# Performance work log

Hardware: AMD Instinct MI355X
Metric: run time of the kernel (lower is better)

## Reference

```python
import jax, jax.numpy as jnp
import numpy as np
import math

B, T, H, W, D = 64, 512, 128, 128, 32


def _lin(k, out, inn):
    k1, k2 = jax.random.split(k)
    lim = 1.0 / np.sqrt(inn)
    return (jax.random.uniform(k1, (out, inn), jnp.float32, -lim, lim),
            jax.random.uniform(k2, (out,), jnp.float32, -lim, lim))


def setup_inputs() -> dict:
    key = jax.random.key(0)
    ks = jax.random.split(key, 12)
    ts = jnp.broadcast_to(jnp.linspace(0.0, 4.0 * math.pi, T, dtype=jnp.float32), (B, T))
    coef = lambda k: jax.random.normal(k, (B, T - 1, D), jnp.float32) * 0.1
    i_W0, i_b0 = _lin(ks[4], W, D)
    i_W1, i_b1 = _lin(ks[5], W, W)
    i_W2, i_b2 = _lin(ks[6], H, W)
    f_W0, f_b0 = _lin(ks[7], W, H)
    f_W1, f_b1 = _lin(ks[8], W, W)
    f_W2, f_b2 = _lin(ks[9], H * D, W)
    l_W, l_b = _lin(ks[10], 1, H)
    return dict(ts=ts,
                coeff_d=coef(ks[0]), coeff_c=coef(ks[1]), coeff_b=coef(ks[2]), coeff_a=coef(ks[3]),
                i_W0=i_W0, i_b0=i_b0, i_W1=i_W1, i_b1=i_b1, i_W2=i_W2, i_b2=i_b2,
                f_W0=f_W0, f_b0=f_b0, f_W1=f_W1, f_b1=f_b1, f_W2=f_W2, f_b2=f_b2,
                l_W=l_W, l_b=l_b)


def reference(ts, coeff_d, coeff_c, coeff_b, coeff_a,
              i_W0, i_b0, i_W1, i_b1, i_W2, i_b2,
              f_W0, f_b0, f_W1, f_b1, f_W2, f_b2,
              l_W, l_b):
    def initial_mlp(x):  # eqx.nn.MLP default: relu hidden, identity final
        x = jax.nn.relu(i_W0 @ x + i_b0)
        x = jax.nn.relu(i_W1 @ x + i_b1)
        return i_W2 @ x + i_b2

    def func_mlp(y):  # softplus hidden, tanh final, reshape (H, D)
        h = jax.nn.softplus(f_W0 @ y + f_b0)
        h = jax.nn.softplus(f_W1 @ h + f_b1)
        return jnp.tanh(f_W2 @ h + f_b2).reshape(H, D)

    def single(ts_i, d, c, b, a):
        dt = ts_i[1] - ts_i[0]
        y0 = initial_mlp(a[0])  # control.evaluate(ts[0]) = a[0] (frac=0 in first interval)

        def deriv(t):  # diffrax CubicInterpolation.derivative
            idx = jnp.clip(jnp.searchsorted(ts_i, t, side='right') - 1, 0, ts_i.shape[0] - 2)
            frac = t - ts_i[idx]
            return b[idx] + frac * (2.0 * c[idx] + frac * 3.0 * d[idx])

        def f(t, y):  # ControlTerm.to_ode() vf_prod with control=dt
            return (func_mlp(y) @ deriv(t)) * dt

        def step(carry, _):  # ralston_step_fn
            t0, y = carry
            k1 = f(t0, y)
            k2 = f(t0 + 0.5 * dt, y + 0.5 * k1)
            k3 = f(t0 + 0.75 * dt, y + 0.75 * k2)
            y1 = (2.0 / 9.0 * k1 + 1.0 / 3.0 * k2 + 4.0 / 9.0 * k3) * dt + y
            return (t0 + dt, y1), y1

        _, ys = jax.lax.scan(step, (ts_i[0], y0), None, length=ts_i.shape[0])
        return jax.nn.sigmoid(ys @ l_W[0] + l_b[0])  # (T,), evolving_out=True

    return jax.vmap(single)(ts, coeff_d, coeff_c, coeff_b, coeff_a)
```

## Files before the change

kernel.cpp:

```cpp
#include <hip/hip_runtime.h>
#include <hip/hip_bf16.h>

#define TT 512
#define BB 64
#define HH 128
#define WW 128
#define DD 32
#define NTHR 512
#define CSTRIDE 16352

#define SMEM_BYTES 86016

typedef __attribute__((ext_vector_type(8))) short short8;
typedef __attribute__((ext_vector_type(4))) float f32x4;

__device__ __forceinline__ float softplus_f(float x) {
    return fmaxf(x, 0.f) + __logf(1.f + __expf(-fabsf(x)));
}
__device__ __forceinline__ float fast_tanh(float x) {
    float ax = fabsf(x);
    float e  = __expf(-2.f * ax);
    float r  = (1.f - e) * __builtin_amdgcn_rcpf(1.f + e);
    return copysignf(r, x);
}
__device__ __forceinline__ short bf16rne(float x) {
    unsigned u = __float_as_uint(x);
    u += 0x7fffu + ((u >> 16) & 1u);
    return (short)(u >> 16);
}
__device__ __forceinline__ void store_l2(unsigned long long* p, unsigned long long v) {
    asm volatile("global_store_dwordx2 %0, %1, off sc0"
                 :: "v"(p), "v"(v) : "memory");
}
__device__ __forceinline__ unsigned long long load_l2_atomic(unsigned long long* p) {
    unsigned long long v;
    asm volatile("global_atomic_add_x2 %0, %1, %2, off sc0\n\t"
                 "s_waitcnt vmcnt(0)"
                 : "=v"(v) : "v"(p), "v"(0ULL) : "memory");
    return v;
}

__global__ __launch_bounds__(NTHR, 2)
void cde_kernel(const float* __restrict__ ts,
                const float* __restrict__ cd, const float* __restrict__ cc,
                const float* __restrict__ cb, const float* __restrict__ ca,
                const float* __restrict__ iW0, const float* __restrict__ ib0,
                const float* __restrict__ iW1, const float* __restrict__ ib1,
                const float* __restrict__ iW2, const float* __restrict__ ib2,
                const float* __restrict__ fW0, const float* __restrict__ fb0,
                const float* __restrict__ fW1, const float* __restrict__ fb1,
                const float* __restrict__ fW2, const float* __restrict__ fb2,
                const float* __restrict__ lW, const float* __restrict__ lb,
                unsigned* __restrict__ xcdctr,
                float* camb,
                unsigned long long* kslow,
                float* __restrict__ out)
{
    extern __shared__ float sm[];
    float* tss    = sm;
    float* ybuf   = tss + TT;
    float* dvec   = ybuf + 128;
    float* scr    = dvec + 96;
    short* ybf    = (short*)(scr + 256);
    short* h1bf   = ybf + 128;
    short* h2bf   = h1bf + 128;
    int*   clm    = (int*)(h2bf + 128);

    const int tid  = threadIdx.x;
    const int lane = tid & 63;
    const int wv   = tid >> 6;
    const int quad = lane >> 4;
    const int qr   = lane & 15;

    if (tid == 0) {
        unsigned xcc;
        asm volatile("s_getreg_b32 %0, hwreg(HW_REG_XCC_ID)" : "=s"(xcc));
        xcc &= 7u;
        unsigned slot = atomicAdd(&xcdctr[xcc], 1u);
        clm[0] = (int)(xcc * 8u + (slot >> 2));
        clm[1] = (int)(slot & 3u);
    }
    __syncthreads();
    const int b = clm[0];
    const int m = clm[1];

    unsigned long long* kfast =
        (unsigned long long*)(camb + (size_t)b * CSTRIDE + 2048);

    const int cg = qr & 3;
    const int ct = (qr >> 2) & 1;
    const int rh = qr >> 3;
    const int dbase = ct * 16 + quad * 4 + rh * 2;

    for (int i = tid; i < TT; i += NTHR) tss[i] = ts[(size_t)b * TT + i];

    short8 afr[4][8];
    #pragma unroll
    for (int gi = 0; gi < 4; ++gi) {
        int g = m * 32 + wv * 4 + gi;
        #pragma unroll
        for (int t = 0; t < 2; ++t)
        #pragma unroll
        for (int K = 0; K < 4; ++K) {
            int row = g * 32 + t * 16 + qr;
            int col = K * 32 + quad * 8;
            const float* src = fW2 + (size_t)row * WW + col;
            short8 v;
            #pragma unroll
            for (int j = 0; j < 8; ++j) v[j] = bf16rne(src[j]);
            afr[gi][t * 4 + K] = v;
        }
    }
    short8 w0f[4], w1f[4];
    #pragma unroll
    for (int K = 0; K < 4; ++K) {
        int row = wv * 16 + qr;
        int col = K * 32 + quad * 8;
        const float* s0 = fW0 + (size_t)row * HH + col;
        const float* s1 = fW1 + (size_t)row * WW + col;
        short8 v0, v1;
        #pragma unroll
        for (int j = 0; j < 8; ++j) { v0[j] = bf16rne(s0[j]); v1[j] = bf16rne(s1[j]); }
        w0f[K] = v0; w1f[K] = v1;
    }
    const float fb0r = fb0[wv * 16 + quad * 4 + cg];
    const float fb1r = fb1[wv * 16 + quad * 4 + cg];
    const int   hrow = m * 32 + wv * 4 + cg;
    const float fb2a = fb2[hrow * 32 + dbase];
    const float fb2b = fb2[hrow * 32 + dbase + 1];

    __syncthreads();

    const float dt = tss[1] - tss[0];
    float t00 = tss[0];
    const size_t cstride = (size_t)CSTRIDE;
    const float* cdb = cd + (size_t)b * cstride;
    const float* ccb = cc + (size_t)b * cstride;
    const float* cbb = cb + (size_t)b * cstride;

    if (tid < HH) {
        const float* a0 = ca + (size_t)b * cstride;
        float acc = ib0[tid];
        #pragma unroll
        for (int k = 0; k < DD; ++k) acc += iW0[tid * DD + k] * a0[k];
        scr[tid] = fmaxf(acc, 0.f);
    }
    __syncthreads();
    if (tid < HH) {
        float acc = ib1[tid];
        for (int k = 0; k < WW; ++k) acc += iW1[tid * WW + k] * scr[k];
        scr[128 + tid] = fmaxf(acc, 0.f);
    }
    __syncthreads();
    float yreg = 0.f, k1r = 0.f, k2r = 0.f;
    if (tid < HH) {
        float acc = ib2[tid];
        for (int k = 0; k < WW; ++k) acc += iW2[tid * WW + k] * scr[128 + k];
        yreg = acc;
        ybuf[tid] = acc;
        ybf[tid]  = bf16rne(acc);
    }
    __syncthreads();

    float lwa = 0.f, lwb = 0.f, lbv = 0.f;
    if (wv == 0) { lwa = lW[lane]; lwb = lW[64 + lane]; lbv = lb[0]; }

    for (int s = 0; s < TT; ++s) {
        if (wv < 3) {
            float tv = t00 + ((wv == 0) ? 0.f : (wv == 1) ? 0.5f : 0.75f) * dt;
            int cnt = 0;
            #pragma unroll
            for (int ch = 0; ch < 8; ++ch)
                cnt += __popcll(__ballot(tss[ch * 64 + lane] <= tv));
            int idx = min(max(cnt - 1, 0), TT - 2);
            if (lane < DD) {
                float frac = tv - tss[idx];
                size_t o = (size_t)idx * DD + lane;
                dvec[wv * 32 + lane] =
                    cbb[o] + frac * (2.f * ccb[o] + frac * 3.f * cdb[o]);
            }
        }

        #pragma unroll 1
        for (int q = 0; q < 3; ++q) {
            const int gen = s * 3 + q + 1;
            const int buf = gen & 1;

            {
                f32x4 aA = {0.f, 0.f, 0.f, 0.f}, aB = {0.f, 0.f, 0.f, 0.f};
                short8 b0 = *(const short8*)(ybf + 0 * 32 + quad * 8);
                short8 b1 = *(const short8*)(ybf + 1 * 32 + quad * 8);
                short8 b2 = *(const short8*)(ybf + 2 * 32 + quad * 8);
                short8 b3 = *(const short8*)(ybf + 3 * 32 + quad * 8);
                aA = __builtin_amdgcn_mfma_f32_16x16x32_bf16(w0f[0], b0, aA, 0, 0, 0);
                aB = __builtin_amdgcn_mfma_f32_16x16x32_bf16(w0f[1], b1, aB, 0, 0, 0);
                aA = __builtin_amdgcn_mfma_f32_16x16x32_bf16(w0f[2], b2, aA, 0, 0, 0);
                aB = __builtin_amdgcn_mfma_f32_16x16x32_bf16(w0f[3], b3, aB, 0, 0, 0);
                f32x4 h = aA + aB;
                if (qr < 4) {
                    float v = (qr & 1) ? ((qr & 2) ? h[3] : h[1])
                                       : ((qr & 2) ? h[2] : h[0]);
                    h1bf[wv * 16 + quad * 4 + qr] = bf16rne(softplus_f(v + fb0r));
                }
            }
            __syncthreads();
            {
                f32x4 aA = {0.f, 0.f, 0.f, 0.f}, aB = {0.f, 0.f, 0.f, 0.f};
                short8 b0 = *(const short8*)(h1bf + 0 * 32 + quad * 8);
                short8 b1 = *(const short8*)(h1bf + 1 * 32 + quad * 8);
                short8 b2 = *(const short8*)(h1bf + 2 * 32 + quad * 8);
                short8 b3 = *(const short8*)(h1bf + 3 * 32 + quad * 8);
                aA = __builtin_amdgcn_mfma_f32_16x16x32_bf16(w1f[0], b0, aA, 0, 0, 0);
                aB = __builtin_amdgcn_mfma_f32_16x16x32_bf16(w1f[1], b1, aB, 0, 0, 0);
                aA = __builtin_amdgcn_mfma_f32_16x16x32_bf16(w1f[2], b2, aA, 0, 0, 0);
                aB = __builtin_amdgcn_mfma_f32_16x16x32_bf16(w1f[3], b3, aB, 0, 0, 0);
                f32x4 h = aA + aB;
                if (qr < 4) {
                    float v = (qr & 1) ? ((qr & 2) ? h[3] : h[1])
                                       : ((qr & 2) ? h[2] : h[0]);
                    h2bf[wv * 16 + quad * 4 + qr] = bf16rne(softplus_f(v + fb1r));
                }
            }
            __syncthreads();
            {
                short8 bfr[4];
                #pragma unroll
                for (int K = 0; K < 4; ++K)
                    bfr[K] = *(const short8*)(h2bf + K * 32 + quad * 8);
                f32x4 A0[4], A1[4];
                #pragma unroll
                for (int gi = 0; gi < 4; ++gi) {
                    f32x4 a0 = {0.f, 0.f, 0.f, 0.f};
                    f32x4 a1 = {0.f, 0.f, 0.f, 0.f};
                    a0 = __builtin_amdgcn_mfma_f32_16x16x32_bf16(afr[gi][0], bfr[0], a0, 0, 0, 0);
                    a0 = __builtin_amdgcn_mfma_f32_16x16x32_bf16(afr[gi][1], bfr[1], a0, 0, 0, 0);
                    a0 = __builtin_amdgcn_mfma_f32_16x16x32_bf16(afr[gi][2], bfr[2], a0, 0, 0, 0);
                    a0 = __builtin_amdgcn_mfma_f32_16x16x32_bf16(afr[gi][3], bfr[3], a0, 0, 0, 0);
                    a1 = __builtin_amdgcn_mfma_f32_16x16x32_bf16(afr[gi][4], bfr[0], a1, 0, 0, 0);
                    a1 = __builtin_amdgcn_mfma_f32_16x16x32_bf16(afr[gi][5], bfr[1], a1, 0, 0, 0);
                    a1 = __builtin_amdgcn_mfma_f32_16x16x32_bf16(afr[gi][6], bfr[2], a1, 0, 0, 0);
                    a1 = __builtin_amdgcn_mfma_f32_16x16x32_bf16(afr[gi][7], bfr[3], a1, 0, 0, 0);
                    A0[gi] = a0; A1[gi] = a1;
                }
                f32x4 s0a = (cg & 1) ? A0[1] : A0[0];
                f32x4 s0b = (cg & 1) ? A0[3] : A0[2];
                f32x4 s0  = (cg & 2) ? s0b : s0a;
                f32x4 s1a = (cg & 1) ? A1[1] : A1[0];
                f32x4 s1b = (cg & 1) ? A1[3] : A1[2];
                f32x4 s1  = (cg & 2) ? s1b : s1a;
                f32x4 st  = ct ? s1 : s0;
                float va = rh ? st[2] : st[0];
                float vb = rh ? st[3] : st[1];
                float2 dv = *(const float2*)(dvec + q * 32 + dbase);
                float p = fast_tanh(va + fb2a) * dv.x + fast_tanh(vb + fb2b) * dv.y;
                p += __shfl_xor(p, 8);
                p += __shfl_xor(p, 4);
                p += __shfl_xor(p, 16);
                p += __shfl_xor(p, 32);
                if (lane < 4) {
                    const float kval = p * dt;
                    const size_t off = (size_t)buf * HH + m * 32 + wv * 4 + lane;
                    unsigned long long pk =
                        ((unsigned long long)__float_as_uint(kval) << 32) | (unsigned)gen;
                    store_l2(kfast + off, pk);
                    __hip_atomic_store(&kslow[(size_t)(buf * BB + b) * HH + m * 32 + wv * 4 + lane],
                                       pk, __ATOMIC_RELAXED, __HIP_MEMORY_SCOPE_AGENT);
                }
            }

            if (tid < HH) {
                unsigned long long* fp = kfast + (size_t)buf * HH + tid;
                unsigned long long v;
                int it = 0;
                for (;;) {
                    if (it < 8 || (it & 1) == 0) {
                        v = load_l2_atomic(fp);
                    } else {
                        v = __hip_atomic_load(&kslow[(size_t)(buf * BB + b) * HH + tid],
                                              __ATOMIC_RELAXED, __HIP_MEMORY_SCOPE_AGENT);
                    }
                    if ((unsigned)v == (unsigned)gen) break;
                    if (++it > 64) __builtin_amdgcn_s_sleep(1);
                }
                float kv = __uint_as_float((unsigned)(v >> 32));
                float nxt;
                if (q == 0)      { k1r = kv; nxt = yreg + 0.5f  * kv; }
                else if (q == 1) { k2r = kv; nxt = yreg + 0.75f * kv; }
                else {
                    nxt = yreg + dt * ((2.f/9.f) * k1r + (1.f/3.f) * k2r + (4.f/9.f) * kv);
                    yreg = nxt;
                    ybuf[tid] = nxt;
                }
                ybf[tid] = bf16rne(nxt);
            }
            __syncthreads();
        }

        if (m == 0 && wv == 0) {
            float p = ybuf[lane] * lwa + ybuf[64 + lane] * lwb;
            p += __shfl_xor(p, 1);  p += __shfl_xor(p, 2);  p += __shfl_xor(p, 4);
            p += __shfl_xor(p, 8);  p += __shfl_xor(p, 16); p += __shfl_xor(p, 32);
            if (lane == 0) out[(size_t)b * TT + s] = 1.f / (1.f + __expf(-(p + lbv)));
        }
        t00 += dt;
    }
}

extern "C" void kernel_launch(void* const* d_in, const int* in_sizes, int n_in,
                              void* d_out, int out_size, void* d_ws, size_t ws_size,
                              hipStream_t stream) {
    const float* ts  = (const float*)d_in[0];
    const float* cdp = (const float*)d_in[1];
    const float* ccp = (const float*)d_in[2];
    const float* cbp = (const float*)d_in[3];
    const float* cap = (const float*)d_in[4];
    const float* iW0 = (const float*)d_in[5];
    const float* ib0 = (const float*)d_in[6];
    const float* iW1 = (const float*)d_in[7];
    const float* ib1 = (const float*)d_in[8];
    const float* iW2 = (const float*)d_in[9];
    const float* ib2 = (const float*)d_in[10];
    const float* fW0 = (const float*)d_in[11];
    const float* fb0 = (const float*)d_in[12];
    const float* fW1 = (const float*)d_in[13];
    const float* fb1 = (const float*)d_in[14];
    const float* fW2 = (const float*)d_in[15];
    const float* fb2 = (const float*)d_in[16];
    const float* lW  = (const float*)d_in[17];
    const float* lb  = (const float*)d_in[18];
    float* out = (float*)d_out;

    unsigned* xcdctr = (unsigned*)d_ws;
    unsigned long long* kslow = (unsigned long long*)((char*)d_ws + 256);
    hipMemsetAsync(d_ws, 0, 256 + (size_t)2 * BB * HH * sizeof(unsigned long long), stream);

    hipFuncSetAttribute((const void*)cde_kernel,
                        hipFuncAttributeMaxDynamicSharedMemorySize, SMEM_BYTES);
    hipLaunchKernelGGL(cde_kernel, dim3(256), dim3(NTHR), SMEM_BYTES, stream,
                       ts, cdp, ccp, cbp, cap, iW0, ib0, iW1, ib1, iW2, ib2,
                       fW0, fb0, fW1, fb1, fW2, fb2, lW, lb, xcdctr,
                       (float*)cap, kslow, out);
}
```

Baseline: 3.606 ms.

## Carry first-layer pre-activation state instead of y and exchange partial projections

The solver state becomes z = W0·y + b0 instead of y. Because z is linear in y, each Ralston stage updates z with W0·k, computed as per-block partial sums over each block's 32-row slice of k. The blocks exchange these partials all-to-all through L2 and poll the three peer slots at once. This removes the first-layer MFMA and its barrier from every stage, and the logistic readout is built the same way by accumulating lW·k partials. In exchange each stage adds a 32-wide fp32 dot, three-way polling with more memory traffic, a new barrier for the local k buffer, and a larger workspace.

```diff
diff --git a/kernel.cpp b/kernel.cpp
--- a/kernel.cpp
+++ b/kernel.cpp
@@ -38,6 +38,13 @@
                  "s_waitcnt vmcnt(0)"
                  : "=v"(v) : "v"(p), "v"(0ULL) : "memory");
     return v;
+}
+__device__ __forceinline__ void probe_issue(unsigned long long* p, unsigned long long& v) {
+    asm volatile("global_atomic_add_x2 %0, %1, %2, off sc0"
+                 : "=v"(v) : "v"(p), "v"(0ULL) : "memory");
+}
+__device__ __forceinline__ void probe_collect(unsigned long long& v) {
+    asm volatile("s_waitcnt vmcnt(0)" : "+v"(v) :: "memory");
 }
 
 __global__ __launch_bounds__(NTHR, 2)
@@ -61,8 +68,8 @@
     float* ybuf   = tss + TT;
     float* dvec   = ybuf + 128;
     float* scr    = dvec + 96;
-    short* ybf    = (short*)(scr + 256);
-    short* h1bf   = ybf + 128;
+    float* klocal = scr + 256;
+    short* h1bf   = (short*)(klocal + 32);
     short* h2bf   = h1bf + 128;
     int*   clm    = (int*)(h2bf + 128);
 
@@ -84,8 +91,10 @@
     const int b = clm[0];
     const int m = clm[1];
 
-    unsigned long long* kfast =
-        (unsigned long long*)(camb + (size_t)b * CSTRIDE + 2048);
+    unsigned long long* ufast = (unsigned long long*)(camb + (size_t)b * CSTRIDE + 2048);
+    unsigned long long* sfast = ufast + (size_t)2 * HH * 4;
+    unsigned long long* umirror = kslow;
+    unsigned long long* smirror = kslow + (size_t)2 * BB * HH * 4;
 
     const int cg = qr & 3;
     const int ct = (qr >> 2) & 1;
@@ -111,23 +120,32 @@
             afr[gi][t * 4 + K] = v;
         }
     }
-    short8 w0f[4], w1f[4];
+    short8 w1f[4];
     #pragma unroll
     for (int K = 0; K < 4; ++K) {
         int row = wv * 16 + qr;
         int col = K * 32 + quad * 8;
-        const float* s0 = fW0 + (size_t)row * HH + col;
         const float* s1 = fW1 + (size_t)row * WW + col;
-        short8 v0, v1;
-        #pragma unroll
-        for (int j = 0; j < 8; ++j) { v0[j] = bf16rne(s0[j]); v1[j] = bf16rne(s1[j]); }
-        w0f[K] = v0; w1f[K] = v1;
-    }
-    const float fb0r = fb0[wv * 16 + quad * 4 + cg];
+        short8 v1;
+        #pragma unroll
+        for (int j = 0; j < 8; ++j) v1[j] = bf16rne(s1[j]);
+        w1f[K] = v1;
+    }
+    float W0s[32];
+    if (tid < HH) {
+        #pragma unroll
+        for (int j = 0; j < 32; ++j) W0s[j] = fW0[(size_t)tid * HH + m * 32 + j];
+    } else {
+        #pragma unroll
+        for (int j = 0; j < 32; ++j) W0s[j] = 0.f;
+    }
     const float fb1r = fb1[wv * 16 + quad * 4 + cg];
     const int   hrow = m * 32 + wv * 4 + cg;
     const float fb2a = fb2[hrow * 32 + dbase];
     const float fb2b = fb2[hrow * 32 + dbase + 1];
+    float lwa = 0.f, lwb = 0.f, lbv = 0.f, lWs = 0.f;
+    if (wv == 3) { lwa = lW[lane]; lwb = lW[64 + lane]; lbv = lb[0]; }
+    if (wv == 7 && lane < 32) lWs = lW[m * 32 + lane];
 
     __syncthreads();
 
@@ -152,18 +170,30 @@
         scr[128 + tid] = fmaxf(acc, 0.f);
     }
     __syncthreads();
-    float yreg = 0.f, k1r = 0.f, k2r = 0.f;
     if (tid < HH) {
         float acc = ib2[tid];
         for (int k = 0; k < WW; ++k) acc += iW2[tid * WW + k] * scr[128 + k];
-        yreg = acc;
         ybuf[tid] = acc;
-        ybf[tid]  = bf16rne(acc);
-    }
-    __syncthreads();
-
-    float lwa = 0.f, lwb = 0.f, lbv = 0.f;
-    if (wv == 0) { lwa = lW[lane]; lwb = lW[64 + lane]; lbv = lb[0]; }
+    }
+    __syncthreads();
+
+    float zb = 0.f, U1r = 0.f, U2r = 0.f;
+    if (tid < HH) {
+        float acc = fb0[tid];
+        for (int k = 0; k < WW; ++k) acc += fW0[(size_t)tid * HH + k] * ybuf[k];
+        zb = acc;
+        h1bf[tid] = bf16rne(softplus_f(acc));
+    }
+    float rreg = 0.f;
+    if (wv == 3) {
+        float p = ybuf[lane] * lwa + ybuf[64 + lane] * lwb;
+        p += __shfl_xor(p, 1);  p += __shfl_xor(p, 2);  p += __shfl_xor(p, 4);
+        p += __shfl_xor(p, 8);  p += __shfl_xor(p, 16); p += __shfl_xor(p, 32);
+        rreg = p + lbv;
+    }
+    __syncthreads();
+
+    const int o0 = (m + 1) & 3, o1 = (m + 2) & 3, o2 = (m + 3) & 3;
 
     for (int s = 0; s < TT; ++s) {
         if (wv < 3) {
@@ -186,24 +216,6 @@
             const int gen = s * 3 + q + 1;
             const int buf = gen & 1;
 
-            {
-                f32x4 aA = {0.f, 0.f, 0.f, 0.f}, aB = {0.f, 0.f, 0.f, 0.f};
-                short8 b0 = *(const short8*)(ybf + 0 * 32 + quad * 8);
-                short8 b1 = *(const short8*)(ybf + 1 * 32 + quad * 8);
-                short8 b2 = *(const short8*)(ybf + 2 * 32 + quad * 8);
-                short8 b3 = *(const short8*)(ybf + 3 * 32 + quad * 8);
-                aA = __builtin_amdgcn_mfma_f32_16x16x32_bf16(w0f[0], b0, aA, 0, 0, 0);
-                aB = __builtin_amdgcn_mfma_f32_16x16x32_bf16(w0f[1], b1, aB, 0, 0, 0);
-                aA = __builtin_amdgcn_mfma_f32_16x16x32_bf16(w0f[2], b2, aA, 0, 0, 0);
-                aB = __builtin_amdgcn_mfma_f32_16x16x32_bf16(w0f[3], b3, aB, 0, 0, 0);
-                f32x4 h = aA + aB;
-                if (qr < 4) {
-                    float v = (qr & 1) ? ((qr & 2) ? h[3] : h[1])
-                                       : ((qr & 2) ? h[2] : h[0]);
-                    h1bf[wv * 16 + quad * 4 + qr] = bf16rne(softplus_f(v + fb0r));
-                }
-            }
-            __syncthreads();
             {
                 f32x4 aA = {0.f, 0.f, 0.f, 0.f}, aB = {0.f, 0.f, 0.f, 0.f};
                 short8 b0 = *(const short8*)(h1bf + 0 * 32 + quad * 8);
@@ -222,6 +234,7 @@
                 }
             }
             __syncthreads();
+
             {
                 short8 bfr[4];
                 #pragma unroll
@@ -257,50 +270,108 @@
                 p += __shfl_xor(p, 4);
                 p += __shfl_xor(p, 16);
                 p += __shfl_xor(p, 32);
-                if (lane < 4) {
-                    const float kval = p * dt;
-                    const size_t off = (size_t)buf * HH + m * 32 + wv * 4 + lane;
+                if (lane < 4) klocal[wv * 4 + lane] = p * dt;
+            }
+            __syncthreads();
+
+            if (wv == 7) {
+                float sp_ = (lane < 32) ? lWs * klocal[lane] : 0.f;
+                sp_ += __shfl_xor(sp_, 1);  sp_ += __shfl_xor(sp_, 2);
+                sp_ += __shfl_xor(sp_, 4);  sp_ += __shfl_xor(sp_, 8);
+                sp_ += __shfl_xor(sp_, 16);
+                if (lane == 0) {
+                    const int qidx = gen % 6;
                     unsigned long long pk =
-                        ((unsigned long long)__float_as_uint(kval) << 32) | (unsigned)gen;
-                    store_l2(kfast + off, pk);
-                    __hip_atomic_store(&kslow[(size_t)(buf * BB + b) * HH + m * 32 + wv * 4 + lane],
-                                       pk, __ATOMIC_RELAXED, __HIP_MEMORY_SCOPE_AGENT);
+                        ((unsigned long long)__float_as_uint(sp_) << 32) | (unsigned)gen;
+                    store_l2(sfast + qidx * 4 + m, pk);
+                    __hip_atomic_store(smirror + ((size_t)qidx * BB + b) * 4 + m, pk,
+                                       __ATOMIC_RELAXED, __HIP_MEMORY_SCOPE_AGENT);
                 }
             }
 
             if (tid < HH) {
-                unsigned long long* fp = kfast + (size_t)buf * HH + tid;
-                unsigned long long v;
-                int it = 0;
+                float ua = 0.f, ub = 0.f, uc = 0.f, ud = 0.f;
+                #pragma unroll
+                for (int i = 0; i < 8; ++i) {
+                    f32x4 kk = *(const f32x4*)(klocal + i * 4);
+                    ua += W0s[i * 4 + 0] * kk[0];
+                    ub += W0s[i * 4 + 1] * kk[1];
+                    uc += W0s[i * 4 + 2] * kk[2];
+                    ud += W0s[i * 4 + 3] * kk[3];
+                }
+                const float uown = (ua + uc) + (ub + ud);
+                unsigned long long pk =
+                    ((unsigned long long)__float_as_uint(uown) << 32) | (unsigned)gen;
+                unsigned long long* ubase = ufast + ((size_t)buf * HH + tid) * 4;
+                unsigned long long* mbase = umirror + (((size_t)buf * BB + b) * HH + tid) * 4;
+                store_l2(ubase + m, pk);
+                __hip_atomic_store(mbase + m, pk,
+                                   __ATOMIC_RELAXED, __HIP_MEMORY_SCOPE_AGENT);
+
+                unsigned long long a0 = 0, a1 = 0, a2 = 0;
+                unsigned done = 0; int it = 0;
                 for (;;) {
-                    if (it < 8 || (it & 1) == 0) {
-                        v = load_l2_atomic(fp);
+                    if (it < 6 || !(it & 1)) {
+                        if (!(done & 1)) probe_issue(ubase + o0, a0);
+                        if (!(done & 2)) probe_issue(ubase + o1, a1);
+                        if (!(done & 4)) probe_issue(ubase + o2, a2);
+                        if (!(done & 1)) probe_collect(a0);
+                        if (!(done & 2)) probe_collect(a1);
+                        if (!(done & 4)) probe_collect(a2);
                     } else {
-                        v = __hip_atomic_load(&kslow[(size_t)(buf * BB + b) * HH + tid],
-                                              __ATOMIC_RELAXED, __HIP_MEMORY_SCOPE_AGENT);
+                        if (!(done & 1)) a0 = __hip_atomic_load(mbase + o0, __ATOMIC_RELAXED, __HIP_MEMORY_SCOPE_AGENT);
+                        if (!(done & 2)) a1 = __hip_atomic_load(mbase + o1, __ATOMIC_RELAXED, __HIP_MEMORY_SCOPE_AGENT);
+                        if (!(done & 4)) a2 = __hip_atomic_load(mbase + o2, __ATOMIC_RELAXED, __HIP_MEMORY_SCOPE_AGENT);
                     }
-                    if ((unsigned)v == (unsigned)gen) break;
+                    if ((unsigned)a0 == (unsigned)gen) done |= 1;
+                    if ((unsigned)a1 == (unsigned)gen) done |= 2;
+                    if ((unsigned)a2 == (unsigned)gen) done |= 4;
+                    if (done == 7u) break;
                     if (++it > 64) __builtin_amdgcn_s_sleep(1);
                 }
-                float kv = __uint_as_float((unsigned)(v >> 32));
-                float nxt;
-                if (q == 0)      { k1r = kv; nxt = yreg + 0.5f  * kv; }
-                else if (q == 1) { k2r = kv; nxt = yreg + 0.75f * kv; }
+                const float U = uown
+                              + __uint_as_float((unsigned)(a0 >> 32))
+                              + __uint_as_float((unsigned)(a1 >> 32))
+                              + __uint_as_float((unsigned)(a2 >> 32));
+                float zs;
+                if (q == 0)      { U1r = U; zs = zb + 0.5f  * U; }
+                else if (q == 1) { U2r = U; zs = zb + 0.75f * U; }
                 else {
-                    nxt = yreg + dt * ((2.f/9.f) * k1r + (1.f/3.f) * k2r + (4.f/9.f) * kv);
-                    yreg = nxt;
-                    ybuf[tid] = nxt;
-                }
-                ybf[tid] = bf16rne(nxt);
+                    zb = zb + dt * ((2.f/9.f) * U1r + (1.f/3.f) * U2r + (4.f/9.f) * U);
+                    zs = zb;
+                }
+                h1bf[tid] = bf16rne(softplus_f(zs));
             }
             __syncthreads();
         }
 
-        if (m == 0 && wv == 0) {
-            float p = ybuf[lane] * lwa + ybuf[64 + lane] * lwb;
-            p += __shfl_xor(p, 1);  p += __shfl_xor(p, 2);  p += __shfl_xor(p, 4);
-            p += __shfl_xor(p, 8);  p += __shfl_xor(p, 16); p += __shfl_xor(p, 32);
-            if (lane == 0) out[(size_t)b * TT + s] = 1.f / (1.f + __expf(-(p + lbv)));
+        if (m == 0 && wv == 3) {
+            float contrib = 0.f;
+            if (lane < 12) {
+                const int qi = lane >> 2, mm = lane & 3;
+                const int geq = s * 3 + qi + 1;
+                const int qidx = geq % 6;
+                unsigned long long* fp  = sfast + qidx * 4 + mm;
+                unsigned long long* mp2 = smirror + ((size_t)qidx * BB + b) * 4 + mm;
+                unsigned long long v; int it = 0;
+                for (;;) {
+                    if (it < 6 || !(it & 1)) v = load_l2_atomic(fp);
+                    else v = __hip_atomic_load(mp2, __ATOMIC_RELAXED, __HIP_MEMORY_SCOPE_AGENT);
+                    if ((unsigned)v == (unsigned)geq) break;
+                    if (++it > 64) __builtin_amdgcn_s_sleep(1);
+                }
+                const float sv = __uint_as_float((unsigned)(v >> 32));
+                const float cf = (qi == 0) ? (2.f/9.f) : (qi == 1) ? (1.f/3.f) : (4.f/9.f);
+                contrib = cf * sv;
+            }
+            contrib += __shfl_xor(contrib, 1);
+            contrib += __shfl_xor(contrib, 2);
+            contrib += __shfl_xor(contrib, 4);
+            contrib += __shfl_xor(contrib, 8);
+            if (lane == 0) {
+                rreg += dt * contrib;
+                out[(size_t)b * TT + s] = 1.f / (1.f + __expf(-rreg));
+            }
         }
         t00 += dt;
     }
@@ -332,7 +403,9 @@
 
     unsigned* xcdctr = (unsigned*)d_ws;
     unsigned long long* kslow = (unsigned long long*)((char*)d_ws + 256);
-    hipMemsetAsync(d_ws, 0, 256 + (size_t)2 * BB * HH * sizeof(unsigned long long), stream);
+    const size_t mirror_bytes =
+        ((size_t)2 * BB * HH * 4 + (size_t)6 * BB * 4) * sizeof(unsigned long long);
+    hipMemsetAsync(d_ws, 0, 256 + mirror_bytes, stream);
 
     hipFuncSetAttribute((const void*)cde_kernel,
                         hipFuncAttributeMaxDynamicSharedMemorySize, SMEM_BYTES);
```

Result: slower. 8.848 ms (+145.4%).
